# Kernel tuning notes

Hardware: AMD Instinct MI355X
Metric: run time of the kernel (lower is better)

The kernel has to match this reference:

```python
import jax, jax.numpy as jnp
import numpy as np

H = 16        # num_attention_heads
KVH = 4       # num_key_value_heads
D = 128       # head_dim
K = 5         # query multiplier k
HID = 2048    # hidden_size = H * D
THETA = 10000.0


def rotate_half(x):
    h = x.shape[-1] // 2
    return jnp.concatenate([-x[..., h:], x[..., :h]], axis=-1)


def setup_inputs() -> dict:
    key = jax.random.key(0)
    ks = jax.random.split(key, 6)
    B, S = 1, 1024
    q_len = S - 1
    hidden_states = jax.random.normal(ks[0], (B, S, HID), jnp.float32)
    prev_hidden_states = jax.random.normal(ks[1], (B, S - 1, HID), jnp.float32)
    causal = jnp.tril(jnp.ones((q_len, q_len), bool))
    attention_mask = jnp.where(causal, 0.0, -1e9).astype(jnp.float32)[None, None]  # (1,1,q,kv)
    position_ids = jnp.arange(q_len, dtype=jnp.int64)[None]  # (1, kv_len)
    Wq = jax.random.normal(ks[2], (HID, H * D * K), jnp.float32) * 0.02
    Wkv = jax.random.normal(ks[3], (2 * HID, 2 * KVH * D), jnp.float32) * 0.02
    Wo = jax.random.normal(ks[4], (HID, HID), jnp.float32) * 0.02
    return {
        'hidden_states': hidden_states,
        'prev_hidden_states': prev_hidden_states,
        'attention_mask': attention_mask,
        'position_ids': position_ids,
        'Wq': Wq,
        'Wkv': Wkv,
        'Wo': Wo,
    }


def reference(hidden_states, prev_hidden_states, attention_mask, position_ids, Wq, Wkv, Wo):
    B = hidden_states.shape[0]  # must be 1 for this module's broadcasting
    # feature-dim concat of previous layer states with shifted current states
    prev = jnp.concatenate([prev_hidden_states, hidden_states[:, :-1]], axis=-1)  # (B, S-1, 2*HID)
    hs = hidden_states[:, 1:]  # training-mode slice -> (B, q_len, HID)
    q_len = hs.shape[1]
    kv_len = prev.shape[1]

    q = hs @ Wq                       # (B, q_len, H*D*K)
    kv = prev @ Wkv                   # (B, kv_len, 2*KVH*D)
    k_st, v_st = jnp.split(kv, 2, axis=-1)

    # faithful raw reshape: (B, q_len, H*D*K) -> (B*K, q_len, H, D) -> (B*K, H, q_len, D)
    q = q.reshape(B * K, -1, H, D).transpose(0, 2, 1, 3)
    k_st = k_st.reshape(B, kv_len, KVH, D).transpose(0, 2, 1, 3)   # (B, KVH, kv, D)
    v_st = v_st.reshape(B, kv_len, KVH, D).transpose(0, 2, 1, 3)

    # RoPE (LlamaRotaryEmbedding)
    inv_freq = 1.0 / (THETA ** (jnp.arange(0, D, 2, dtype=jnp.float32) / D))  # (D/2,)
    freqs = position_ids.astype(jnp.float32)[..., None] * inv_freq            # (B, kv, D/2)
    emb = jnp.concatenate([freqs, freqs], axis=-1)                            # (B, kv, D)
    cos = jnp.cos(emb)[:, None]  # (B, 1, kv, D)
    sin = jnp.sin(emb)[:, None]
    q = q * cos[..., -q_len:, :] + rotate_half(q) * sin[..., -q_len:, :]
    k_st = k_st * cos[..., :kv_len, :] + rotate_half(k_st) * sin[..., :kv_len, :]

    # repeat_kv: (B, KVH, kv, D) -> (B, H, kv, D)
    n_rep = H // KVH
    k_rep = jnp.repeat(k_st, n_rep, axis=1)
    v_rep = jnp.repeat(v_st, n_rep, axis=1)

    # (B*K, H, q, D) @ (B, H, D, kv) -> broadcast over k variants (B==1)
    attn = jnp.matmul(q, jnp.swapaxes(k_rep, -1, -2)) / jnp.sqrt(jnp.float32(D))
    attn = attn + attention_mask
    attn = jax.nn.softmax(attn.astype(jnp.float32), axis=-1).astype(q.dtype)
    out = jnp.matmul(attn, v_rep)                 # (B*K, H, q, D)
    out = out.transpose(0, 2, 1, 3).reshape(B * K, q_len, HID)
    return out @ Wo                                # (B*K, q_len, HID)
```

## Files before the change

### kernel.cpp

```cpp
#include <hip/hip_runtime.h>
#include <cstddef>
#include <cstdint>

#define SQ    1023
#define HIDC  2048
#define NQC   10240
#define NKVC  1024

typedef unsigned short ushort_t;
typedef __bf16 bf16x8 __attribute__((ext_vector_type(8)));
typedef float  f32x4  __attribute__((ext_vector_type(4)));

__device__ __forceinline__ ushort_t f2bf(float x) {
  union { float f; uint32_t u; } v; v.f = x;
  uint32_t r = v.u + 0x7fffu + ((v.u >> 16) & 1u);
  return (ushort_t)(r >> 16);
}

__device__ __forceinline__ ushort_t f2bf_fast(float x) {
  __bf16 b = (__bf16)x;
  return __builtin_bit_cast(ushort_t, b);
}

__device__ __forceinline__ float fexp2(float x) {
  float r;
  asm("v_exp_f32 %0, %1\n\ts_nop 0" : "=v"(r) : "v"(x));
  return r;
}

__device__ __forceinline__ void fexp2x4(float& a, float& b, float& c, float& d) {
  asm("v_exp_f32 %0, %0\n\t"
      "v_exp_f32 %1, %1\n\t"
      "v_exp_f32 %2, %2\n\t"
      "v_exp_f32 %3, %3\n\t"
      "s_nop 0"
      : "+v"(a), "+v"(b), "+v"(c), "+v"(d));
}

__device__ __forceinline__ void tconv_body(const float* __restrict__ in,
                                           ushort_t* __restrict__ out,
                                           int K, int N, int bx, int by,
                                           int tid, float (&t)[32][33]) {
  int n0 = bx * 32, k0 = by * 32;
  int r = tid >> 5, c = tid & 31;
  #pragma unroll
  for (int p = 0; p < 4; ++p)
    t[p * 8 + r][c] = in[(size_t)(k0 + p * 8 + r) * N + n0 + c];
  __syncthreads();
  #pragma unroll
  for (int p = 0; p < 4; ++p)
    out[(size_t)(n0 + p * 8 + r) * K + k0 + c] = f2bf(t[c][p * 8 + r]);
}

__global__ __launch_bounds__(256)
void k_pre(const float* __restrict__ Wq, const float* __restrict__ Wkv,
           const float* __restrict__ Wo, const float* __restrict__ hidden,
           const float* __restrict__ prevh,
           ushort_t* __restrict__ wqt, ushort_t* __restrict__ wkvt,
           ushort_t* __restrict__ wot, ushort_t* __restrict__ hbf,
           ushort_t* __restrict__ akv,
           float* __restrict__ cosT, float* __restrict__ sinT)
{
  __shared__ float tsh[32][33];
  const int tid = threadIdx.x;
  int b = blockIdx.x;
  if (b < 20480) { tconv_body(Wq, wqt, HIDC, NQC, b % 320, b / 320, tid, tsh); return; }
  b -= 20480;
  if (b < 4096)  { tconv_body(Wkv, wkvt, 4096, NKVC, b % 32, b / 32, tid, tsh); return; }
  b -= 4096;
  if (b < 4096)  { tconv_body(Wo, wot, HIDC, HIDC, b % 64, b / 64, tid, tsh); return; }
  b -= 4096;
  if (b < 2046) {
    int i = (b * 256 + tid) * 4;
    if (i >= SQ * 2048) return;
    int r = i >> 11, c = i & 2047;
    float4 h1 = *reinterpret_cast<const float4*>(hidden + (size_t)(r + 1) * 2048 + c);
    float4 h0 = *reinterpret_cast<const float4*>(hidden + (size_t)r * 2048 + c);
    float4 pv = *reinterpret_cast<const float4*>(prevh + (size_t)r * 2048 + c);
    uint2 a, bb, d;
    a.x  = (uint32_t)f2bf(h1.x) | ((uint32_t)f2bf(h1.y) << 16);
    a.y  = (uint32_t)f2bf(h1.z) | ((uint32_t)f2bf(h1.w) << 16);
    bb.x = (uint32_t)f2bf(pv.x) | ((uint32_t)f2bf(pv.y) << 16);
    bb.y = (uint32_t)f2bf(pv.z) | ((uint32_t)f2bf(pv.w) << 16);
    d.x  = (uint32_t)f2bf(h0.x) | ((uint32_t)f2bf(h0.y) << 16);
    d.y  = (uint32_t)f2bf(h0.z) | ((uint32_t)f2bf(h0.w) << 16);
    *reinterpret_cast<uint2*>(hbf + i) = a;
    *reinterpret_cast<uint2*>(akv + (size_t)r * 4096 + c) = bb;
    *reinterpret_cast<uint2*>(akv + (size_t)r * 4096 + 2048 + c) = d;
    return;
  }
  b -= 2046;
  {
    int idx = b * 256 + tid;
    if (idx >= SQ * 64) return;
    int t = idx >> 6, i = idx & 63;
    float inv = powf(10000.0f, -(float)i * (1.0f / 64.0f));
    float f = (float)t * inv;
    cosT[idx] = cosf(f);
    sinT[idx] = sinf(f);
  }
}

__global__ __launch_bounds__(256)
void k_gemms(const ushort_t* __restrict__ hbf, const ushort_t* __restrict__ wqt,
             ushort_t* __restrict__ qbb, const float* __restrict__ cosT,
             const float* __restrict__ sinT,
             const ushort_t* __restrict__ akv, const ushort_t* __restrict__ wkvt,
             float* __restrict__ kvp)
{
  __shared__ __align__(16) ushort_t As[3][128 * 32];
  __shared__ __align__(16) ushort_t Bs[3][128 * 32];

  const int tid  = threadIdx.x;
  const int lane = tid & 63;
  const int w    = tid >> 6;
  const int wm   = w >> 1, wn = w & 1;
  const int fr   = lane & 15;
  const int kg   = (lane >> 4) * 8;
  const int g4   = lane >> 4;
  const int lrow = lane >> 2;
  const int lk   = (lane & 3) * 8;

  if (blockIdx.x < 640) {
    const int Kd = 2048;
    const int m0 = (blockIdx.x / 80) * 128, n0 = (blockIdx.x % 80) * 128;
    const ushort_t* A  = hbf;
    const ushort_t* Bt = wqt;

    f32x4 acc[4][4];
    #pragma unroll
    for (int i = 0; i < 4; ++i)
      #pragma unroll
      for (int j = 0; j < 4; ++j) acc[i][j] = (f32x4){0.f, 0.f, 0.f, 0.f};

    auto STAGE = [&](int b, int k0) {
      #pragma unroll
      for (int c = 0; c < 2; ++c) {
        int ch  = w + c * 4;
        int row = ch * 16 + lrow;
        const ushort_t* ga = A  + (size_t)(m0 + row) * Kd + k0 + lk;
        const ushort_t* gb = Bt + (size_t)(n0 + row) * Kd + k0 + lk;
        __builtin_amdgcn_global_load_lds(
            (const __attribute__((address_space(1))) void*)ga,
            (__attribute__((address_space(3))) void*)(&As[b][0] + ch * 512), 16, 0, 0);
        __builtin_amdgcn_global_load_lds(
            (const __attribute__((address_space(1))) void*)gb,
            (__attribute__((address_space(3))) void*)(&Bs[b][0] + ch * 512), 16, 0, 0);
      }
    };

    const int nt = Kd / 32;
    STAGE(0, 0);
    STAGE(1, 32);

    int cur = 0;
    for (int t = 0; t < nt; ++t) {
      if (t + 1 < nt) {
        asm volatile("s_waitcnt vmcnt(4)" ::: "memory");
      } else {
        asm volatile("s_waitcnt vmcnt(0)" ::: "memory");
      }
      __builtin_amdgcn_s_barrier();
      if (t + 2 < nt) {
        int sb = cur + 2; if (sb >= 3) sb -= 3;
        STAGE(sb, (t + 2) * 32);
      }

      bf16x8 av[4], bv[4];
      #pragma unroll
      for (int mi = 0; mi < 4; ++mi)
        av[mi] = *reinterpret_cast<const bf16x8*>(&As[cur][0] + (wm * 64 + mi * 16 + fr) * 32 + kg);
      #pragma unroll
      for (int nj = 0; nj < 4; ++nj) {
        int colOff = wn * 32 + (nj & 1) * 16 + (nj >> 1) * 64;
        bv[nj] = *reinterpret_cast<const bf16x8*>(&Bs[cur][0] + (colOff + fr) * 32 + kg);
      }
      #pragma unroll
      for (int mi = 0; mi < 4; ++mi)
        #pragma unroll
        for (int nj = 0; nj < 4; ++nj)
          acc[mi][nj] = __builtin_amdgcn_mfma_f32_16x16x32_bf16(av[mi], bv[nj], acc[mi][nj], 0, 0, 0);

      cur = (cur == 2) ? 0 : cur + 1;
    }

    const float sc = 0.1275174485f;
    const int nChunk = n0 >> 11;
    #pragma unroll
    for (int mi = 0; mi < 4; ++mi) {
      #pragma unroll
      for (int r = 0; r < 4; ++r) {
        int gr = m0 + wm * 64 + mi * 16 + g4 * 4 + r;
        if (gr >= SQ) continue;
        int st  = gr * 5 + nChunk;
        int tau = st % 1023;
        const float* ct  = cosT + tau * 64;
        const float* stb = sinT + tau * 64;
        #pragma unroll
        for (int njp = 0; njp < 2; ++njp) {
          int dd = wn * 32 + njp * 16 + fr;
          float c = ct[dd], s = stb[dd];
          float x0 = acc[mi][njp][r];
          float x1 = acc[mi][njp + 2][r];
          size_t base = (size_t)gr * 10240 + n0 + dd;
          qbb[base]      = f2bf_fast((x0 * c - x1 * s) * sc);
          qbb[base + 64] = f2bf_fast((x1 * c + x0 * s) * sc);
        }
      }
    }
  } else {
    const int u = blockIdx.x - 640;
    const int Kd = 4096, M = SQ, N = NKVC, kLen = 1024;
    const int n0 = (u & 7) * 128, m0 = ((u >> 3) & 15) * 64;
    const int kOff = (u >> 7) * kLen;
    float* C = kvp + (size_t)(u >> 7) * M * N;
    ushort_t* As64 = &As[0][0];
    ushort_t* Bs64 = &Bs[0][0];

    const int arow = tid >> 2, aslot = (tid & 3) * 8;
    const int l15 = lane & 15;

    f32x4 acc[2][4];
    #pragma unroll
    for (int i = 0; i < 2; ++i)
      #pragma unroll
      for (int j = 0; j < 4; ++j) acc[i][j] = (f32x4){0.f, 0.f, 0.f, 0.f};

    for (int k0 = kOff; k0 < kOff + kLen; k0 += 32) {
      {
        const ushort_t* ga = akv + (size_t)(m0 + arow) * Kd + k0 + aslot;
        __builtin_amdgcn_global_load_lds(
            (const __attribute__((address_space(1))) void*)ga,
            (__attribute__((address_space(3))) void*)(As64 + w * 512), 16, 0, 0);
      }
      #pragma unroll
      for (int c = 0; c < 2; ++c) {
        int uu = c * 256 + tid;
        const ushort_t* gb = wkvt + (size_t)(n0 + (uu >> 2)) * Kd + k0 + (uu & 3) * 8;
        __builtin_amdgcn_global_load_lds(
            (const __attribute__((address_space(1))) void*)gb,
            (__attribute__((address_space(3))) void*)(Bs64 + (c * 256 + w * 64) * 8), 16, 0, 0);
      }
      __syncthreads();

      bf16x8 av[2], bv[4];
      #pragma unroll
      for (int mi = 0; mi < 2; ++mi)
        av[mi] = *reinterpret_cast<const bf16x8*>(As64 + (wm * 32 + mi * 16 + fr) * 32 + kg);
      #pragma unroll
      for (int nj = 0; nj < 4; ++nj)
        bv[nj] = *reinterpret_cast<const bf16x8*>(Bs64 + (wn * 64 + nj * 16 + fr) * 32 + kg);
      #pragma unroll
      for (int mi = 0; mi < 2; ++mi)
        #pragma unroll
        for (int nj = 0; nj < 4; ++nj)
          acc[mi][nj] = __builtin_amdgcn_mfma_f32_16x16x32_bf16(av[mi], bv[nj], acc[mi][nj], 0, 0, 0);
      __syncthreads();
    }

    #pragma unroll
    for (int mi = 0; mi < 2; ++mi) {
      #pragma unroll
      for (int nj = 0; nj < 4; ++nj) {
        int rbase = m0 + wm * 32 + mi * 16 + g4 * 4;
        int col   = n0 + wn * 64 + nj * 16 + l15;
        #pragma unroll
        for (int r = 0; r < 4; ++r) {
          int gr = rbase + r;
          if (gr < M) C[(size_t)gr * N + col] = acc[mi][nj][r];
        }
      }
    }
  }
}

__global__ __launch_bounds__(256)
void k_kv(const float* __restrict__ kvp, ushort_t* __restrict__ kb,
          ushort_t* __restrict__ vt, const float* __restrict__ cosT,
          const float* __restrict__ sinT)
{
  __shared__ float tile[32][33];
  const int tid = threadIdx.x;
  int b = blockIdx.x;
  if (b < 1023) {
    int idx = b * 256 + tid;
    if (idx >= SQ * 4 * 64) return;
    int d   = idx & 63;
    int kvh = (idx >> 6) & 3;
    int t   = idx >> 8;
    size_t src = (size_t)t * 1024 + kvh * 128 + d;
    float x0 = 0.f, x1 = 0.f;
    #pragma unroll
    for (int z = 0; z < 4; ++z) {
      x0 += kvp[(size_t)z * (SQ * 1024) + src];
      x1 += kvp[(size_t)z * (SQ * 1024) + src + 64];
    }
    float c = cosT[t * 64 + d], s = sinT[t * 64 + d];
    size_t dst = (size_t)t * 512 + kvh * 128 + d;
    kb[dst]      = f2bf(x0 * c - x1 * s);
    kb[dst + 64] = f2bf(x1 * c + x0 * s);
    return;
  }
  b -= 1023;
  {
    int v0 = (b & 15) * 32;
    int t0 = (b >> 4) * 32;
    int r = tid >> 5, c = tid & 31;
    #pragma unroll
    for (int p = 0; p < 4; ++p) {
      int t = t0 + p * 8 + r;
      float s = 0.f;
      if (t < SQ) {
        size_t src = (size_t)t * 1024 + 512 + v0 + c;
        #pragma unroll
        for (int z = 0; z < 4; ++z) s += kvp[(size_t)z * (SQ * 1024) + src];
      }
      tile[p * 8 + r][c] = s;
    }
    __syncthreads();
    #pragma unroll
    for (int p = 0; p < 4; ++p) {
      int v = v0 + p * 8 + r;
      vt[(size_t)v * 1024 + t0 + c] = f2bf(tile[c][p * 8 + r]);
    }
  }
}

__global__ __launch_bounds__(256)
void k_gemm3buf(const ushort_t* __restrict__ A, const ushort_t* __restrict__ Bt,
                float* __restrict__ C, int M, int N, int Kd)
{
  __shared__ __align__(16) ushort_t As[3][128 * 32];
  __shared__ __align__(16) ushort_t Bs[3][128 * 32];

  const int tid  = threadIdx.x;
  const int lane = tid & 63;
  const int w    = tid >> 6;
  const int wm   = w >> 1, wn = w & 1;
  const int fr   = lane & 15;
  const int kg   = (lane >> 4) * 8;
  const int m0   = blockIdx.y * 128, n0 = blockIdx.x * 128;

  const int lrow = lane >> 2;
  const int lk   = (lane & 3) * 8;

  f32x4 acc[4][4];
  #pragma unroll
  for (int i = 0; i < 4; ++i)
    #pragma unroll
    for (int j = 0; j < 4; ++j) acc[i][j] = (f32x4){0.f, 0.f, 0.f, 0.f};

  auto STAGE = [&](int b, int k0) {
    #pragma unroll
    for (int c = 0; c < 2; ++c) {
      int ch  = w + c * 4;
      int row = ch * 16 + lrow;
      const ushort_t* ga = A  + (size_t)(m0 + row) * Kd + k0 + lk;
      const ushort_t* gb = Bt + (size_t)(n0 + row) * Kd + k0 + lk;
      __builtin_amdgcn_global_load_lds(
          (const __attribute__((address_space(1))) void*)ga,
          (__attribute__((address_space(3))) void*)(&As[b][0] + ch * 512), 16, 0, 0);
      __builtin_amdgcn_global_load_lds(
          (const __attribute__((address_space(1))) void*)gb,
          (__attribute__((address_space(3))) void*)(&Bs[b][0] + ch * 512), 16, 0, 0);
    }
  };

  const int nt = Kd / 32;
  STAGE(0, 0);
  STAGE(1, 32);

  int cur = 0;
  for (int t = 0; t < nt; ++t) {
    if (t + 1 < nt) {
      asm volatile("s_waitcnt vmcnt(4)" ::: "memory");
    } else {
      asm volatile("s_waitcnt vmcnt(0)" ::: "memory");
    }
    __builtin_amdgcn_s_barrier();
    if (t + 2 < nt) {
      int sb = cur + 2; if (sb >= 3) sb -= 3;
      STAGE(sb, (t + 2) * 32);
    }

    bf16x8 av[4], bv[4];
    #pragma unroll
    for (int mi = 0; mi < 4; ++mi)
      av[mi] = *reinterpret_cast<const bf16x8*>(&As[cur][0] + (wm * 64 + mi * 16 + fr) * 32 + kg);
    #pragma unroll
    for (int nj = 0; nj < 4; ++nj)
      bv[nj] = *reinterpret_cast<const bf16x8*>(&Bs[cur][0] + (wn * 64 + nj * 16 + fr) * 32 + kg);
    #pragma unroll
    for (int mi = 0; mi < 4; ++mi)
      #pragma unroll
      for (int nj = 0; nj < 4; ++nj)
        acc[mi][nj] = __builtin_amdgcn_mfma_f32_16x16x32_bf16(av[mi], bv[nj], acc[mi][nj], 0, 0, 0);

    cur = (cur == 2) ? 0 : cur + 1;
  }

  #pragma unroll
  for (int mi = 0; mi < 4; ++mi) {
    #pragma unroll
    for (int nj = 0; nj < 4; ++nj) {
      int rbase = m0 + wm * 64 + mi * 16 + (lane >> 4) * 4;
      int col   = n0 + wn * 64 + nj * 16 + fr;
      #pragma unroll
      for (int r = 0; r < 4; ++r) {
        int gr = rbase + r;
        if (gr < M) C[(size_t)gr * N + col] = acc[mi][nj][r];
      }
    }
  }
}

__global__ __launch_bounds__(256)
void k_attn_mfma(const ushort_t* __restrict__ qb, const ushort_t* __restrict__ kb,
                 const ushort_t* __restrict__ vt, ushort_t* __restrict__ oattb)
{
  __shared__ __align__(16) ushort_t Ks[64 * 128];
  __shared__ __align__(16) ushort_t Vs[128 * 64];
  __shared__ __align__(16) ushort_t Ps[4][16 * 64];

  const int tid  = threadIdx.x;
  const int lane = tid & 63;
  const int w    = tid >> 6;
  const int l15  = lane & 15;
  const int g4   = lane >> 4;
  const int gh   = blockIdx.x;
  const int g = gh >> 4, h = gh & 15, kvh = (gh & 15) >> 2;
  const int qt = 15 - blockIdx.y;
  const int t0 = qt * 64;

  bf16x8 av[4];
  {
    int t = t0 + w * 16 + l15;
    const ushort_t* qrow = qb + (((size_t)(g * SQ + t)) * 16 + h) * 128;
    #pragma unroll
    for (int kk = 0; kk < 4; ++kk)
      av[kk] = *reinterpret_cast<const bf16x8*>(qrow + kk * 32 + g4 * 8);
  }

  bf16x8 ones;
  #pragma unroll
  for (int j = 0; j < 8; ++j) ones[j] = __builtin_bit_cast(__bf16, (ushort_t)0x3F80);

  f32x4 acc[8];
  #pragma unroll
  for (int dt = 0; dt < 8; ++dt) acc[dt] = (f32x4){0.f, 0.f, 0.f, 0.f};
  f32x4 acc_l = (f32x4){0.f, 0.f, 0.f, 0.f};
  float m[4];
  #pragma unroll
  for (int r = 0; r < 4; ++r) m[r] = -1e30f;

  ushort_t* pw = &Ps[w][0];

  for (int jt = 0; jt <= qt; ++jt) {
    int u0 = jt * 64;
    #pragma unroll
    for (int i = 0; i < 4; ++i) {
      int c = (w * 4 + i) * 64 + lane;
      int kv = c >> 4, sl = c & 15;
      const ushort_t* srck = kb + (size_t)(u0 + kv) * 512 + kvh * 128 + ((sl ^ (kv & 7)) << 3);
      __builtin_amdgcn_global_load_lds(
          (const __attribute__((address_space(1))) void*)srck,
          (__attribute__((address_space(3))) void*)(Ks + (w * 4 + i) * 512), 16, 0, 0);
      int d = c >> 3, sv = c & 7;
      const ushort_t* srcv = vt + (size_t)(kvh * 128 + d) * 1024 + u0 + ((sv ^ (d & 7)) << 3);
      __builtin_amdgcn_global_load_lds(
          (const __attribute__((address_space(1))) void*)srcv,
          (__attribute__((address_space(3))) void*)(Vs + (w * 4 + i) * 512), 16, 0, 0);
    }
    __syncthreads();

    f32x4 S[4];
    #pragma unroll
    for (int ct = 0; ct < 4; ++ct) S[ct] = (f32x4){0.f, 0.f, 0.f, 0.f};
    #pragma unroll
    for (int ct = 0; ct < 4; ++ct) {
      int kv = ct * 16 + l15;
      #pragma unroll
      for (int kk = 0; kk < 4; ++kk) {
        bf16x8 bv = *reinterpret_cast<const bf16x8*>(
            Ks + kv * 128 + ((((kk << 2) | g4) ^ (kv & 7)) << 3));
        S[ct] = __builtin_amdgcn_mfma_f32_16x16x32_bf16(av[kk], bv, S[ct], 0, 0, 0);
      }
    }
    if (jt == qt) {
      #pragma unroll
      for (int ct = 0; ct < 4; ++ct) {
        int u = u0 + ct * 16 + l15;
        #pragma unroll
        for (int r = 0; r < 4; ++r) {
          int t = t0 + w * 16 + g4 * 4 + r;
          if (u > t) S[ct][r] = -1e30f;
        }
      }
    }
    float tm[4];
    #pragma unroll
    for (int r = 0; r < 4; ++r) {
      float t1 = fmaxf(fmaxf(S[0][r], S[1][r]), fmaxf(S[2][r], S[3][r]));
      t1 = fmaxf(t1, __shfl_xor(t1, 1));
      t1 = fmaxf(t1, __shfl_xor(t1, 2));
      t1 = fmaxf(t1, __shfl_xor(t1, 4));
      t1 = fmaxf(t1, __shfl_xor(t1, 8));
      tm[r] = t1;
    }
    bool need = (tm[0] > m[0] + 8.f) || (tm[1] > m[1] + 8.f) ||
                (tm[2] > m[2] + 8.f) || (tm[3] > m[3] + 8.f);
    if (__any(need)) {
      #pragma unroll
      for (int r = 0; r < 4; ++r) {
        float mn = fmaxf(m[r], tm[r]);
        float corr = fexp2(m[r] - mn);
        m[r] = mn;
        acc_l[r] *= corr;
        #pragma unroll
        for (int dt = 0; dt < 8; ++dt) acc[dt][r] *= corr;
      }
    }
    #pragma unroll
    for (int r = 0; r < 4; ++r) {
      float e0 = S[0][r] - m[r];
      float e1 = S[1][r] - m[r];
      float e2 = S[2][r] - m[r];
      float e3 = S[3][r] - m[r];
      fexp2x4(e0, e1, e2, e3);
      S[0][r] = e0; S[1][r] = e1; S[2][r] = e2; S[3][r] = e3;
    }

    #pragma unroll
    for (int ct = 0; ct < 4; ++ct) {
      int kv = ct * 16 + l15;
      #pragma unroll
      for (int r = 0; r < 4; ++r) {
        int q = g4 * 4 + r;
        pw[q * 64 + ((((kv >> 3) ^ (q & 7)) << 3) | (kv & 7))] = f2bf_fast(S[ct][r]);
      }
    }
    #pragma unroll
    for (int kk = 0; kk < 2; ++kk) {
      bf16x8 pa = *reinterpret_cast<const bf16x8*>(
          pw + l15 * 64 + ((((kk << 2) | g4) ^ (l15 & 7)) << 3));
      acc_l = __builtin_amdgcn_mfma_f32_16x16x32_bf16(pa, ones, acc_l, 0, 0, 0);
      #pragma unroll
      for (int dt = 0; dt < 8; ++dt) {
        int d = dt * 16 + l15;
        bf16x8 vv = *reinterpret_cast<const bf16x8*>(
            Vs + d * 64 + ((((kk << 2) | g4) ^ (d & 7)) << 3));
        acc[dt] = __builtin_amdgcn_mfma_f32_16x16x32_bf16(pa, vv, acc[dt], 0, 0, 0);
      }
    }
    __syncthreads();
  }

  #pragma unroll
  for (int r = 0; r < 4; ++r) {
    int t = t0 + w * 16 + g4 * 4 + r;
    if (t >= SQ) continue;
    float inv = 1.f / acc_l[r];
    ushort_t* dst = oattb + ((size_t)(g * SQ + t)) * 2048 + h * 128;
    #pragma unroll
    for (int dt = 0; dt < 8; ++dt)
      dst[dt * 16 + l15] = f2bf_fast(acc[dt][r] * inv);
  }
}

extern "C" void kernel_launch(void* const* d_in, const int* in_sizes, int n_in,
                              void* d_out, int out_size, void* d_ws, size_t ws_size,
                              hipStream_t stream) {
  const float* hidden = (const float*)d_in[0];
  const float* prevh  = (const float*)d_in[1];
  const float* Wq     = (const float*)d_in[4];
  const float* Wkv    = (const float*)d_in[5];
  const float* Wo     = (const float*)d_in[6];
  float* out = (float*)d_out;

  char* ws = (char*)d_ws;
  float*    kvp   = (float*)ws;                        ws += (size_t)4 * SQ * 1024 * 4;
  float*    cosT  = (float*)ws;                        ws += (size_t)65472 * 4;
  float*    sinT  = (float*)ws;                        ws += (size_t)65472 * 4;
  ushort_t* qbb   = (ushort_t*)ws;                     ws += (size_t)5120 * 2048 * 2;
  ushort_t* kb    = (ushort_t*)ws;                     ws += (size_t)1024 * 512 * 2;
  ushort_t* vtb   = (ushort_t*)ws;                     ws += (size_t)512 * 1024 * 2;
  ushort_t* hbf   = (ushort_t*)ws;                     ws += (size_t)1024 * 2048 * 2;
  ushort_t* akv   = (ushort_t*)ws;                     ws += (size_t)1024 * 4096 * 2;
  ushort_t* oattb = (ushort_t*)ws;                     ws += (size_t)5120 * 2048 * 2;
  ushort_t* wqt   = (ushort_t*)ws;                     ws += (size_t)10240 * 2048 * 2;
  ushort_t* wkvt  = (ushort_t*)ws;                     ws += (size_t)1024 * 4096 * 2;
  ushort_t* wot   = (ushort_t*)ws;                     ws += (size_t)2048 * 2048 * 2;

  k_pre<<<dim3(20480 + 4096 + 4096 + 2046 + 256), dim3(256), 0, stream>>>(
      Wq, Wkv, Wo, hidden, prevh, wqt, wkvt, wot, hbf, akv, cosT, sinT);

  k_gemms<<<dim3(1152), dim3(256), 0, stream>>>(
      hbf, wqt, qbb, cosT, sinT, akv, wkvt, kvp);

  k_kv<<<dim3(1023 + 512), dim3(256), 0, stream>>>(kvp, kb, vtb, cosT, sinT);

  k_attn_mfma<<<dim3(80, 16), dim3(256), 0, stream>>>(qbb, kb, vtb, oattb);

  k_gemm3buf<<<dim3(HIDC / 128, 40), dim3(256), 0, stream>>>(oattb, wot, out, 5115, HIDC, 2048);
}
```

Measured before the change: 245.6 us.

## Transpose attention MFMA operands so each lane owns one query row

The attention kernel swaps the A/B operands of both MFMAs, computing S^T and O^T so that each lane holds one query row's values across its four accumulator registers. This turns the row max and row sum into in-register reductions plus two cross-lane shuffles, and drops the extra ones-vector MFMA that computed the softmax denominator. P is written to LDS as packed 8-byte stores and the output as packed bf16 pairs instead of scalar stores. The row-sum is now taken from fp32 exponentials rather than their bf16-rounded values, which slightly changes numerics.

After: 244.0 us (median of 2 runs). Within noise of the previous version (-0.7%).

```diff
diff --git a/kernel.cpp b/kernel.cpp
--- a/kernel.cpp
+++ b/kernel.cpp
@@ -431,29 +431,24 @@
   const int g = gh >> 4, h = gh & 15, kvh = (gh & 15) >> 2;
   const int qt = 15 - blockIdx.y;
   const int t0 = qt * 64;
+  const int tq = t0 + w * 16 + l15;
 
   bf16x8 av[4];
   {
-    int t = t0 + w * 16 + l15;
-    const ushort_t* qrow = qb + (((size_t)(g * SQ + t)) * 16 + h) * 128;
+    const ushort_t* qrow = qb + (((size_t)(g * SQ + tq)) * 16 + h) * 128;
     #pragma unroll
     for (int kk = 0; kk < 4; ++kk)
       av[kk] = *reinterpret_cast<const bf16x8*>(qrow + kk * 32 + g4 * 8);
   }
-
-  bf16x8 ones;
-  #pragma unroll
-  for (int j = 0; j < 8; ++j) ones[j] = __builtin_bit_cast(__bf16, (ushort_t)0x3F80);
 
   f32x4 acc[8];
   #pragma unroll
   for (int dt = 0; dt < 8; ++dt) acc[dt] = (f32x4){0.f, 0.f, 0.f, 0.f};
-  f32x4 acc_l = (f32x4){0.f, 0.f, 0.f, 0.f};
-  float m[4];
-  #pragma unroll
-  for (int r = 0; r < 4; ++r) m[r] = -1e30f;
-
-  ushort_t* pw = &Ps[w][0];
+  float lsum = 0.f;
+  float m = -1e30f;
+
+  char* pwb = (char*)&Ps[w][0] + l15 * 128;
+  const int pswz = (l15 & 7) << 4;
 
   for (int jt = 0; jt <= qt; ++jt) {
     int u0 = jt * 64;
@@ -481,89 +476,80 @@
       int kv = ct * 16 + l15;
       #pragma unroll
       for (int kk = 0; kk < 4; ++kk) {
-        bf16x8 bv = *reinterpret_cast<const bf16x8*>(
+        bf16x8 kvf = *reinterpret_cast<const bf16x8*>(
             Ks + kv * 128 + ((((kk << 2) | g4) ^ (kv & 7)) << 3));
-        S[ct] = __builtin_amdgcn_mfma_f32_16x16x32_bf16(av[kk], bv, S[ct], 0, 0, 0);
+        S[ct] = __builtin_amdgcn_mfma_f32_16x16x32_bf16(kvf, av[kk], S[ct], 0, 0, 0);
       }
     }
     if (jt == qt) {
       #pragma unroll
       for (int ct = 0; ct < 4; ++ct) {
-        int u = u0 + ct * 16 + l15;
+        int ub = u0 + ct * 16 + g4 * 4;
         #pragma unroll
-        for (int r = 0; r < 4; ++r) {
-          int t = t0 + w * 16 + g4 * 4 + r;
-          if (u > t) S[ct][r] = -1e30f;
-        }
-      }
-    }
-    float tm[4];
-    #pragma unroll
-    for (int r = 0; r < 4; ++r) {
-      float t1 = fmaxf(fmaxf(S[0][r], S[1][r]), fmaxf(S[2][r], S[3][r]));
-      t1 = fmaxf(t1, __shfl_xor(t1, 1));
-      t1 = fmaxf(t1, __shfl_xor(t1, 2));
-      t1 = fmaxf(t1, __shfl_xor(t1, 4));
-      t1 = fmaxf(t1, __shfl_xor(t1, 8));
-      tm[r] = t1;
-    }
-    bool need = (tm[0] > m[0] + 8.f) || (tm[1] > m[1] + 8.f) ||
-                (tm[2] > m[2] + 8.f) || (tm[3] > m[3] + 8.f);
+        for (int r = 0; r < 4; ++r)
+          if (ub + r > tq) S[ct][r] = -1e30f;
+      }
+    }
+    float a0 = fmaxf(fmaxf(S[0][0], S[0][1]), fmaxf(S[0][2], S[0][3]));
+    float a1 = fmaxf(fmaxf(S[1][0], S[1][1]), fmaxf(S[1][2], S[1][3]));
+    float a2 = fmaxf(fmaxf(S[2][0], S[2][1]), fmaxf(S[2][2], S[2][3]));
+    float a3 = fmaxf(fmaxf(S[3][0], S[3][1]), fmaxf(S[3][2], S[3][3]));
+    float tm = fmaxf(fmaxf(a0, a1), fmaxf(a2, a3));
+    tm = fmaxf(tm, __shfl_xor(tm, 16));
+    tm = fmaxf(tm, __shfl_xor(tm, 32));
+
+    bool need = tm > m + 8.f;
     if (__any(need)) {
-      #pragma unroll
-      for (int r = 0; r < 4; ++r) {
-        float mn = fmaxf(m[r], tm[r]);
-        float corr = fexp2(m[r] - mn);
-        m[r] = mn;
-        acc_l[r] *= corr;
-        #pragma unroll
-        for (int dt = 0; dt < 8; ++dt) acc[dt][r] *= corr;
-      }
-    }
-    #pragma unroll
-    for (int r = 0; r < 4; ++r) {
-      float e0 = S[0][r] - m[r];
-      float e1 = S[1][r] - m[r];
-      float e2 = S[2][r] - m[r];
-      float e3 = S[3][r] - m[r];
+      float mn = fmaxf(m, tm);
+      float corr = fexp2(m - mn);
+      m = mn;
+      lsum *= corr;
+      #pragma unroll
+      for (int dt = 0; dt < 8; ++dt) acc[dt] *= corr;
+    }
+
+    float ps = 0.f;
+    #pragma unroll
+    for (int ct = 0; ct < 4; ++ct) {
+      float e0 = S[ct][0] - m;
+      float e1 = S[ct][1] - m;
+      float e2 = S[ct][2] - m;
+      float e3 = S[ct][3] - m;
       fexp2x4(e0, e1, e2, e3);
-      S[0][r] = e0; S[1][r] = e1; S[2][r] = e2; S[3][r] = e3;
-    }
-
-    #pragma unroll
-    for (int ct = 0; ct < 4; ++ct) {
-      int kv = ct * 16 + l15;
-      #pragma unroll
-      for (int r = 0; r < 4; ++r) {
-        int q = g4 * 4 + r;
-        pw[q * 64 + ((((kv >> 3) ^ (q & 7)) << 3) | (kv & 7))] = f2bf_fast(S[ct][r]);
-      }
-    }
+      ps += (e0 + e1) + (e2 + e3);
+      uint2 pv;
+      pv.x = (uint32_t)f2bf_fast(e0) | ((uint32_t)f2bf_fast(e1) << 16);
+      pv.y = (uint32_t)f2bf_fast(e2) | ((uint32_t)f2bf_fast(e3) << 16);
+      *reinterpret_cast<uint2*>(pwb + ((ct * 32 + g4 * 8) ^ pswz)) = pv;
+    }
+    ps += __shfl_xor(ps, 16);
+    ps += __shfl_xor(ps, 32);
+    lsum += ps;
+
     #pragma unroll
     for (int kk = 0; kk < 2; ++kk) {
-      bf16x8 pa = *reinterpret_cast<const bf16x8*>(
-          pw + l15 * 64 + ((((kk << 2) | g4) ^ (l15 & 7)) << 3));
-      acc_l = __builtin_amdgcn_mfma_f32_16x16x32_bf16(pa, ones, acc_l, 0, 0, 0);
+      bf16x8 pa = *reinterpret_cast<const bf16x8*>(pwb + ((kk * 64 + g4 * 16) ^ pswz));
       #pragma unroll
       for (int dt = 0; dt < 8; ++dt) {
         int d = dt * 16 + l15;
         bf16x8 vv = *reinterpret_cast<const bf16x8*>(
             Vs + d * 64 + ((((kk << 2) | g4) ^ (d & 7)) << 3));
-        acc[dt] = __builtin_amdgcn_mfma_f32_16x16x32_bf16(pa, vv, acc[dt], 0, 0, 0);
+        acc[dt] = __builtin_amdgcn_mfma_f32_16x16x32_bf16(vv, pa, acc[dt], 0, 0, 0);
       }
     }
     __syncthreads();
   }
 
-  #pragma unroll
-  for (int r = 0; r < 4; ++r) {
-    int t = t0 + w * 16 + g4 * 4 + r;
-    if (t >= SQ) continue;
-    float inv = 1.f / acc_l[r];
-    ushort_t* dst = oattb + ((size_t)(g * SQ + t)) * 2048 + h * 128;
-    #pragma unroll
-    for (int dt = 0; dt < 8; ++dt)
-      dst[dt * 16 + l15] = f2bf_fast(acc[dt][r] * inv);
+  if (tq < SQ) {
+    float inv = 1.f / lsum;
+    ushort_t* dst = oattb + ((size_t)(g * SQ + tq)) * 2048 + h * 128;
+    #pragma unroll
+    for (int dt = 0; dt < 8; ++dt) {
+      uint2 ov;
+      ov.x = (uint32_t)f2bf_fast(acc[dt][0] * inv) | ((uint32_t)f2bf_fast(acc[dt][1] * inv) << 16);
+      ov.y = (uint32_t)f2bf_fast(acc[dt][2] * inv) | ((uint32_t)f2bf_fast(acc[dt][3] * inv) << 16);
+      *reinterpret_cast<uint2*>(dst + dt * 16 + g4 * 4) = ov;
+    }
   }
 }
 
```
